# Kernel optimization log

Hardware: AMD Instinct MI355X
Metric: run time of the kernel (lower is better)

The kernel has to match this reference:

```python
import jax, jax.numpy as jnp
import numpy as np

N = 100000
E = 1600000
IN_DIM, HID, NCLS = 512, 64, 16


def setup_inputs() -> dict:
    key = jax.random.key(0)
    ks = jax.random.split(key, 6)
    x = jax.random.normal(ks[0], (N, IN_DIM), dtype=jnp.float32)
    edge_index = jax.random.randint(ks[1], (2, E), 0, N, dtype=jnp.int32)
    edge_weight = jax.random.uniform(ks[2], (E,), dtype=jnp.float32)
    W1 = jax.random.normal(ks[3], (IN_DIM, HID), dtype=jnp.float32) / np.sqrt(IN_DIM)
    b1 = jnp.zeros((HID,), dtype=jnp.float32)
    W2 = jax.random.normal(ks[4], (HID, NCLS), dtype=jnp.float32) / np.sqrt(HID)
    b2 = jnp.zeros((NCLS,), dtype=jnp.float32)
    return {"x": x, "edge_index": edge_index, "edge_weight": edge_weight,
            "W1": W1, "b1": b1, "W2": W2, "b2": b2}


def _gcn_norm(edge_index, edge_weight, num_nodes):
    # PyG GCNConv: add self-loops (weight 1), symmetric deg^-1/2 normalization.
    loop = jnp.arange(num_nodes, dtype=edge_index.dtype)
    src = jnp.concatenate([edge_index[0], loop])
    dst = jnp.concatenate([edge_index[1], loop])
    w = jnp.concatenate([edge_weight, jnp.ones((num_nodes,), edge_weight.dtype)])
    deg = jax.ops.segment_sum(w, dst, num_segments=num_nodes)  # degree at target
    dis = jnp.where(deg > 0, jax.lax.rsqrt(jnp.where(deg > 0, deg, 1.0)), 0.0)
    norm = dis[src] * w * dis[dst]
    return src, dst, norm


def _gcn_layer(x, src, dst, norm, W, b):
    h = x @ W                                   # [N, out]
    msg = h[src] * norm[:, None]                # gather + scale  [E+N, out]
    out = jax.ops.segment_sum(msg, dst, num_segments=x.shape[0])
    return out + b


def reference(x, edge_index, edge_weight, W1, b1, W2, b2):
    src, dst, norm = _gcn_norm(edge_index, edge_weight, x.shape[0])
    h = _gcn_layer(x, src, dst, norm, W1, b1)
    h = jax.nn.relu(h)
    # F.dropout in eval mode is identity (reference assumes inference).
    h = _gcn_layer(h, src, dst, norm, W2, b2)
    return jax.nn.log_softmax(h, axis=-1)
```

## Files before the change

kernel.cpp:

```cpp
#include <hip/hip_runtime.h>
#include <hip/hip_bf16.h>

#define N_NODES 100000
#define N_EDGES 1600000
#define IN_DIM 512
#define HID 64
#define NCLS 16
#define NB ((N_NODES + 1023) / 1024)

typedef __attribute__((ext_vector_type(8))) short bf16x8;
typedef __attribute__((ext_vector_type(8))) unsigned short ushort8;
typedef __attribute__((ext_vector_type(4))) float f32x4;

static __device__ __forceinline__ unsigned short f2bf(float f) {
    union { float f; unsigned int u; } v; v.f = f;
    unsigned int u = v.u;
    unsigned int r = (u + 0x7fffu + ((u >> 16) & 1u)) >> 16;
    return (unsigned short)r;
}
static __device__ __forceinline__ float bf2f(unsigned short u) {
    union { unsigned int i; float f; } v; v.i = ((unsigned int)u) << 16; return v.f;
}


__global__ void k_init(int* cnt) {
    int i = blockIdx.x * 256 + threadIdx.x;
    if (i < N_NODES) cnt[i] = 0;
}

__global__ void k_pass1(const int* __restrict__ dst, int* cnt, int* __restrict__ li) {
    int e = blockIdx.x * 256 + threadIdx.x;
    if (e < N_EDGES) li[e] = atomicAdd(&cnt[dst[e]], 1);
}

__global__ void k_scan1(const int* __restrict__ cnt, int* ptr, int* bsum) {
    __shared__ int s[256];
    int t = threadIdx.x;
    int i0 = blockIdx.x * 1024 + t * 4;
    int c[4];
#pragma unroll
    for (int j = 0; j < 4; j++) c[j] = (i0 + j < N_NODES) ? cnt[i0 + j] : 0;
    int sum4 = c[0] + c[1] + c[2] + c[3];
    s[t] = sum4;
    __syncthreads();
    int v = sum4;
    for (int off = 1; off < 256; off <<= 1) {
        int add = (t >= off) ? s[t - off] : 0;
        __syncthreads();
        v += add;
        s[t] = v;
        __syncthreads();
    }
    int run = v - sum4;
#pragma unroll
    for (int j = 0; j < 4; j++) {
        if (i0 + j < N_NODES) ptr[i0 + j] = run;
        run += c[j];
    }
    if (t == 255) bsum[blockIdx.x] = v;
}

__global__ void k_scan2(int* bsum, int* ptr) {
    __shared__ int s[128];
    int t = threadIdx.x;
    int val = (t < NB) ? bsum[t] : 0;
    s[t] = val;
    __syncthreads();
    int v = val;
    for (int off = 1; off < 128; off <<= 1) {
        int add = (t >= off) ? s[t - off] : 0;
        __syncthreads();
        v += add;
        s[t] = v;
        __syncthreads();
    }
    if (t < NB) bsum[t] = v - val;
    if (t == 0) ptr[N_NODES] = N_EDGES;
}

__global__ void k_scan3(int* ptr, const int* __restrict__ bsum) {
    int t = threadIdx.x;
    int i0 = blockIdx.x * 1024 + t * 4;
    int add = bsum[blockIdx.x];
#pragma unroll
    for (int j = 0; j < 4; j++)
        if (i0 + j < N_NODES) ptr[i0 + j] += add;
}

__global__ void k_pass2(const int* __restrict__ src, const int* __restrict__ dst,
                        const float* __restrict__ w, const int* __restrict__ ptr,
                        const int* __restrict__ li,
                        int* __restrict__ csr_src, float* __restrict__ csr_w) {
    int e = blockIdx.x * 256 + threadIdx.x;
    if (e < N_EDGES) {
        int p = ptr[dst[e]] + li[e];
        csr_src[p] = src[e];
        csr_w[p] = w[e];
    }
}

__global__ void k_degsum(const int* __restrict__ ptr, const float* __restrict__ csr_w,
                         float* __restrict__ dis) {
    int v = blockIdx.x * 256 + threadIdx.x;
    if (v < N_NODES) {
        int p0 = ptr[v], p1 = ptr[v + 1];
        float s = 1.0f;
        for (int p = p0; p < p1; p++) s += csr_w[p];
        dis[v] = rsqrtf(s);
    }
}

__global__ void k_scale(const int* __restrict__ ptr, const int* __restrict__ csr_src,
                        float* __restrict__ csr_w, const float* __restrict__ dis) {
    int v = blockIdx.x * 256 + threadIdx.x;
    if (v < N_NODES) {
        float dv = dis[v];
        int p0 = ptr[v], p1 = ptr[v + 1];
        for (int p = p0; p < p1; p++)
            csr_w[p] = csr_w[p] * dv * dis[csr_src[p]];
    }
}


__global__ void k_prep_w1(const float* __restrict__ W1, unsigned short* __restrict__ wt) {
    int t = blockIdx.x * 256 + threadIdx.x;
    if (t < HID * IN_DIM) {
        int n = t >> 9, k = t & 511;
        wt[t] = f2bf(W1[(size_t)k * HID + n]);
    }
}


#define LDK 72

__global__ __launch_bounds__(256) void k_gemm1(const float* __restrict__ x,
                                               const unsigned short* __restrict__ wt,
                                               unsigned short* __restrict__ h1b) {
    __shared__ unsigned short xs[64][LDK];
    __shared__ unsigned short ws[64][LDK];

    int t = threadIdx.x;
    int row0 = blockIdx.x * 64;
    int wave = t >> 6, lane = t & 63;
    int lm = lane & 15, quad = lane >> 4;

    f32x4 acc[4];
#pragma unroll
    for (int nt = 0; nt < 4; nt++) acc[nt] = (f32x4)(0.f);

    for (int k0 = 0; k0 < IN_DIM; k0 += 64) {
        __syncthreads();
        {
            int c8 = (t & 7) * 8;
#pragma unroll
            for (int h = 0; h < 2; h++) {
                int r = (t >> 3) + h * 32;
                int gr = row0 + r;
                if (gr >= N_NODES) gr = N_NODES - 1;
                const float* xp = x + (size_t)gr * IN_DIM + k0 + c8;
                float4 v0 = *(const float4*)xp;
                float4 v1 = *(const float4*)(xp + 4);
                ushort8 pk;
                pk.s0 = f2bf(v0.x); pk.s1 = f2bf(v0.y); pk.s2 = f2bf(v0.z); pk.s3 = f2bf(v0.w);
                pk.s4 = f2bf(v1.x); pk.s5 = f2bf(v1.y); pk.s6 = f2bf(v1.z); pk.s7 = f2bf(v1.w);
                *(ushort8*)&xs[r][c8] = pk;
            }
        }
        {
            int n = t >> 2, kc = (t & 3) * 16;
            const unsigned short* wp = wt + (size_t)n * IN_DIM + k0 + kc;
            *(ushort8*)&ws[n][kc]     = *(const ushort8*)wp;
            *(ushort8*)&ws[n][kc + 8] = *(const ushort8*)(wp + 8);
        }
        __syncthreads();
#pragma unroll
        for (int kk = 0; kk < 64; kk += 32) {
            bf16x8 afrag = *(bf16x8*)&xs[wave * 16 + lm][kk + quad * 8];
#pragma unroll
            for (int nt = 0; nt < 4; nt++) {
                bf16x8 bfrag = *(bf16x8*)&ws[nt * 16 + lm][kk + quad * 8];
                acc[nt] = __builtin_amdgcn_mfma_f32_16x16x32_bf16(afrag, bfrag, acc[nt], 0, 0, 0);
            }
        }
    }
#pragma unroll
    for (int nt = 0; nt < 4; nt++) {
#pragma unroll
        for (int i = 0; i < 4; i++) {
            int gr = row0 + wave * 16 + quad * 4 + i;
            if (gr < N_NODES) h1b[(size_t)gr * HID + nt * 16 + lm] = f2bf(acc[nt][i]);
        }
    }
}


__global__ __launch_bounds__(256) void k_agg1(const unsigned short* __restrict__ h1b,
                                              const int* __restrict__ ptr,
                                              const int* __restrict__ csr_src,
                                              const float* __restrict__ csr_w,
                                              const float* __restrict__ dis,
                                              const float* __restrict__ b1,
                                              float* __restrict__ a1) {
    int wave = threadIdx.x >> 6, lane = threadIdx.x & 63;
    int v = blockIdx.x * 4 + wave;
    if (v >= N_NODES) return;
    int j = lane >> 4, c = lane & 15;
    int p0 = ptr[v], p1 = ptr[v + 1];

    float a0 = 0.f, a1r = 0.f, a2 = 0.f, a3 = 0.f;
    for (int base = p0; base < p1; base += 8) {
#pragma unroll
        for (int half = 0; half < 2; half++) {
            int idx = base + half * 4 + j;
            bool valid = idx < p1;
            int s = valid ? csr_src[idx] : v;
            float wgt = valid ? csr_w[idx] : 0.f;
            ushort4 g = *(const ushort4*)&h1b[(size_t)s * HID + c * 4];
            a0 += wgt * bf2f(g.x);
            a1r += wgt * bf2f(g.y);
            a2 += wgt * bf2f(g.z);
            a3 += wgt * bf2f(g.w);
        }
    }
#pragma unroll
    for (int m = 16; m <= 32; m <<= 1) {
        a0 += __shfl_xor(a0, m, 64);
        a1r += __shfl_xor(a1r, m, 64);
        a2 += __shfl_xor(a2, m, 64);
        a3 += __shfl_xor(a3, m, 64);
    }
    if (lane < 16) {
        float dv = dis[v], dvv = dv * dv;
        ushort4 sv = *(const ushort4*)&h1b[(size_t)v * HID + c * 4];
        float4 bv = *(const float4*)&b1[c * 4];
        float r0 = a0 + dvv * bf2f(sv.x) + bv.x;
        float r1 = a1r + dvv * bf2f(sv.y) + bv.y;
        float r2 = a2 + dvv * bf2f(sv.z) + bv.z;
        float r3 = a3 + dvv * bf2f(sv.w) + bv.w;
        float4 o;
        o.x = r0 > 0.f ? r0 : 0.f;
        o.y = r1 > 0.f ? r1 : 0.f;
        o.z = r2 > 0.f ? r2 : 0.f;
        o.w = r3 > 0.f ? r3 : 0.f;
        *(float4*)&a1[(size_t)v * HID + c * 4] = o;
    }
}


__global__ __launch_bounds__(256) void k_gemm2(const float* __restrict__ a1,
                                               const float* __restrict__ W2,
                                               float* __restrict__ h2) {
    __shared__ float ws[HID * NCLS];
    for (int i = threadIdx.x; i < HID * NCLS; i += 256) ws[i] = W2[i];
    __syncthreads();
    int t = blockIdx.x * 256 + threadIdx.x;
    int v = t >> 4, c = t & 15;
    if (v >= N_NODES) return;
    const float* row = a1 + (size_t)v * HID;
    float acc = 0.f;
#pragma unroll
    for (int k = 0; k < HID; k += 4) {
        float4 av = *(const float4*)(row + k);
        acc = fmaf(av.x, ws[(k + 0) * NCLS + c], acc);
        acc = fmaf(av.y, ws[(k + 1) * NCLS + c], acc);
        acc = fmaf(av.z, ws[(k + 2) * NCLS + c], acc);
        acc = fmaf(av.w, ws[(k + 3) * NCLS + c], acc);
    }
    h2[(size_t)v * NCLS + c] = acc;
}


__global__ __launch_bounds__(256) void k_agg2(const float* __restrict__ h2,
                                              const int* __restrict__ ptr,
                                              const int* __restrict__ csr_src,
                                              const float* __restrict__ csr_w,
                                              const float* __restrict__ dis,
                                              const float* __restrict__ b2,
                                              float* __restrict__ out) {
    int t = blockIdx.x * 256 + threadIdx.x;
    int v = t >> 4, c = t & 15;
    if (v >= N_NODES) return;
    float dv = dis[v];
    float acc = h2[(size_t)v * NCLS + c] * dv * dv;
    int p0 = ptr[v], p1 = ptr[v + 1];
    int p = p0;
    int n4 = p0 + ((p1 - p0) & ~3);
    for (; p < n4; p += 4) {
        int s0 = csr_src[p], s1 = csr_src[p + 1], s2 = csr_src[p + 2], s3 = csr_src[p + 3];
        float w0 = csr_w[p], w1 = csr_w[p + 1], w2 = csr_w[p + 2], w3 = csr_w[p + 3];
        float g0 = h2[(size_t)s0 * NCLS + c];
        float g1 = h2[(size_t)s1 * NCLS + c];
        float g2 = h2[(size_t)s2 * NCLS + c];
        float g3 = h2[(size_t)s3 * NCLS + c];
        acc += w0 * g0 + w1 * g1 + w2 * g2 + w3 * g3;
    }
    for (; p < p1; p++)
        acc += csr_w[p] * h2[(size_t)csr_src[p] * NCLS + c];
    acc += b2[c];
    float m = acc;
#pragma unroll
    for (int off = 8; off >= 1; off >>= 1) m = fmaxf(m, __shfl_xor(m, off, 16));
    float e = expf(acc - m);
    float s = e;
#pragma unroll
    for (int off = 8; off >= 1; off >>= 1) s += __shfl_xor(s, off, 16);
    out[(size_t)v * NCLS + c] = acc - m - logf(s);
}


extern "C" void kernel_launch(void* const* d_in, const int* in_sizes, int n_in,
                              void* d_out, int out_size, void* d_ws, size_t ws_size,
                              hipStream_t stream) {
    const float* x  = (const float*)d_in[0];
    const int*   ei = (const int*)d_in[1];
    const float* w  = (const float*)d_in[2];
    const float* W1 = (const float*)d_in[3];
    const float* b1 = (const float*)d_in[4];
    const float* W2 = (const float*)d_in[5];
    const float* b2 = (const float*)d_in[6];
    const int* src = ei;
    const int* dst = ei + N_EDGES;

    char* wsb = (char*)d_ws;
    size_t off = 0;
    auto alloc = [&](size_t bytes) {
        void* p = wsb + off;
        off += (bytes + 255) & ~(size_t)255;
        return p;
    };
    int*   cnt   = (int*)  alloc((size_t)N_NODES * 4);
    int*   li    = (int*)  alloc((size_t)N_EDGES * 4);
    int*   ptr   = (int*)  alloc((size_t)(N_NODES + 1) * 4);
    int*   bsum  = (int*)  alloc((size_t)NB * 4);
    int*   csr_s = (int*)  alloc((size_t)N_EDGES * 4);
    float* csr_w = (float*)alloc((size_t)N_EDGES * 4);
    float* dis   = (float*)alloc((size_t)N_NODES * 4);
    unsigned short* h1b = (unsigned short*)alloc((size_t)N_NODES * HID * 2);
    float* a1    = (float*)alloc((size_t)N_NODES * HID * 4);
    float* h2    = (float*)alloc((size_t)N_NODES * NCLS * 4);
    unsigned short* wt = (unsigned short*)alloc((size_t)HID * IN_DIM * 2);

    float* outp = (float*)d_out;

    k_init   <<<(N_NODES + 255) / 256, 256, 0, stream>>>(cnt);
    k_pass1  <<<(N_EDGES + 255) / 256, 256, 0, stream>>>(dst, cnt, li);
    k_scan1  <<<NB, 256, 0, stream>>>(cnt, ptr, bsum);
    k_scan2  <<<1, 128, 0, stream>>>(bsum, ptr);
    k_scan3  <<<NB, 256, 0, stream>>>(ptr, bsum);
    k_pass2  <<<(N_EDGES + 255) / 256, 256, 0, stream>>>(src, dst, w, ptr, li, csr_s, csr_w);
    k_degsum <<<(N_NODES + 255) / 256, 256, 0, stream>>>(ptr, csr_w, dis);
    k_scale  <<<(N_NODES + 255) / 256, 256, 0, stream>>>(ptr, csr_s, csr_w, dis);
    k_prep_w1<<<(HID * IN_DIM + 255) / 256, 256, 0, stream>>>(W1, wt);
    k_gemm1  <<<(N_NODES + 63) / 64, 256, 0, stream>>>(x, wt, h1b);
    k_agg1   <<<(N_NODES + 3) / 4, 256, 0, stream>>>(h1b, ptr, csr_s, csr_w, dis, b1, a1);
    k_gemm2  <<<(N_NODES * NCLS + 255) / 256, 256, 0, stream>>>(a1, W2, h2);
    k_agg2   <<<(N_NODES * NCLS + 255) / 256, 256, 0, stream>>>(h2, ptr, csr_s, csr_w, dis, b2, outp);
}
```

Before: 579.8 us.

## Fold symmetric normalization into features and fuse GEMM2 into layer-1 aggregation

Drops the per-edge k_scale pass by pre-scaling node features by deg^-1/2 in the GEMM epilogues and applying the destination factor after aggregation. The second linear layer is fused into the layer-1 aggregation kernel through an LDS-resident transposed W2 and shuffle reductions, so the fp32 a1 intermediate is never written. Layer-2 features are stored as bf16 and aggregated with the same wave-per-node scheme as layer 1. This cuts memory traffic and one kernel launch, but adds bf16 rounding on h2 and more shuffle work in k_agg1.

```diff
diff --git a/kernel.cpp b/kernel.cpp
--- a/kernel.cpp
+++ b/kernel.cpp
@@ -110,17 +110,6 @@
     }
 }
 
-__global__ void k_scale(const int* __restrict__ ptr, const int* __restrict__ csr_src,
-                        float* __restrict__ csr_w, const float* __restrict__ dis) {
-    int v = blockIdx.x * 256 + threadIdx.x;
-    if (v < N_NODES) {
-        float dv = dis[v];
-        int p0 = ptr[v], p1 = ptr[v + 1];
-        for (int p = p0; p < p1; p++)
-            csr_w[p] = csr_w[p] * dv * dis[csr_src[p]];
-    }
-}
-
 
 __global__ void k_prep_w1(const float* __restrict__ W1, unsigned short* __restrict__ wt) {
     int t = blockIdx.x * 256 + threadIdx.x;
@@ -135,7 +124,8 @@
 
 __global__ __launch_bounds__(256) void k_gemm1(const float* __restrict__ x,
                                                const unsigned short* __restrict__ wt,
-                                               unsigned short* __restrict__ h1b) {
+                                               const float* __restrict__ dis,
+                                               unsigned short* __restrict__ h1s) {
     __shared__ unsigned short xs[64][LDK];
     __shared__ unsigned short ws[64][LDK];
 
@@ -184,30 +174,40 @@
         }
     }
 #pragma unroll
-    for (int nt = 0; nt < 4; nt++) {
-#pragma unroll
-        for (int i = 0; i < 4; i++) {
-            int gr = row0 + wave * 16 + quad * 4 + i;
-            if (gr < N_NODES) h1b[(size_t)gr * HID + nt * 16 + lm] = f2bf(acc[nt][i]);
-        }
-    }
-}
-
-
-__global__ __launch_bounds__(256) void k_agg1(const unsigned short* __restrict__ h1b,
+    for (int i = 0; i < 4; i++) {
+        int gr = row0 + wave * 16 + quad * 4 + i;
+        if (gr < N_NODES) {
+            float dv = dis[gr];
+#pragma unroll
+            for (int nt = 0; nt < 4; nt++)
+                h1s[(size_t)gr * HID + nt * 16 + lm] = f2bf(dv * acc[nt][i]);
+        }
+    }
+}
+
+
+__global__ __launch_bounds__(256) void k_agg1(const unsigned short* __restrict__ h1s,
                                               const int* __restrict__ ptr,
                                               const int* __restrict__ csr_src,
                                               const float* __restrict__ csr_w,
                                               const float* __restrict__ dis,
                                               const float* __restrict__ b1,
-                                              float* __restrict__ a1) {
+                                              const float* __restrict__ W2,
+                                              unsigned short* __restrict__ h2s) {
+    __shared__ float w2t[NCLS * 68];
+    for (int i = threadIdx.x; i < HID * NCLS; i += 256) {
+        int k = i >> 4, cc = i & 15;
+        w2t[cc * 68 + k] = W2[i];
+    }
+    __syncthreads();
+
     int wave = threadIdx.x >> 6, lane = threadIdx.x & 63;
     int v = blockIdx.x * 4 + wave;
     if (v >= N_NODES) return;
     int j = lane >> 4, c = lane & 15;
     int p0 = ptr[v], p1 = ptr[v + 1];
 
-    float a0 = 0.f, a1r = 0.f, a2 = 0.f, a3 = 0.f;
+    float a0 = 0.f, a1v = 0.f, a2 = 0.f, a3 = 0.f;
     for (int base = p0; base < p1; base += 8) {
 #pragma unroll
         for (int half = 0; half < 2; half++) {
@@ -215,9 +215,9 @@
             bool valid = idx < p1;
             int s = valid ? csr_src[idx] : v;
             float wgt = valid ? csr_w[idx] : 0.f;
-            ushort4 g = *(const ushort4*)&h1b[(size_t)s * HID + c * 4];
+            ushort4 g = *(const ushort4*)&h1s[(size_t)s * HID + c * 4];
             a0 += wgt * bf2f(g.x);
-            a1r += wgt * bf2f(g.y);
+            a1v += wgt * bf2f(g.y);
             a2 += wgt * bf2f(g.z);
             a3 += wgt * bf2f(g.w);
         }
@@ -225,86 +225,81 @@
 #pragma unroll
     for (int m = 16; m <= 32; m <<= 1) {
         a0 += __shfl_xor(a0, m, 64);
-        a1r += __shfl_xor(a1r, m, 64);
+        a1v += __shfl_xor(a1v, m, 64);
         a2 += __shfl_xor(a2, m, 64);
         a3 += __shfl_xor(a3, m, 64);
     }
+    float dv = dis[v];
+    ushort4 sv = *(const ushort4*)&h1s[(size_t)v * HID + c * 4];
+    float4 bv = *(const float4*)&b1[c * 4];
+    float r0 = dv * (a0 + bf2f(sv.x)) + bv.x;
+    float r1 = dv * (a1v + bf2f(sv.y)) + bv.y;
+    float r2 = dv * (a2 + bf2f(sv.z)) + bv.z;
+    float r3 = dv * (a3 + bf2f(sv.w)) + bv.w;
+    r0 = r0 > 0.f ? r0 : 0.f;
+    r1 = r1 > 0.f ? r1 : 0.f;
+    r2 = r2 > 0.f ? r2 : 0.f;
+    r3 = r3 > 0.f ? r3 : 0.f;
+
+    float partial[NCLS];
+#pragma unroll
+    for (int cc = 0; cc < NCLS; cc++) {
+        const float* wp = &w2t[cc * 68 + 4 * c];
+        partial[cc] = r0 * wp[0] + r1 * wp[1] + r2 * wp[2] + r3 * wp[3];
+    }
+#pragma unroll
+    for (int m = 1; m <= 8; m <<= 1)
+#pragma unroll
+        for (int cc = 0; cc < NCLS; cc++)
+            partial[cc] += __shfl_xor(partial[cc], m, 16);
+
     if (lane < 16) {
-        float dv = dis[v], dvv = dv * dv;
-        ushort4 sv = *(const ushort4*)&h1b[(size_t)v * HID + c * 4];
-        float4 bv = *(const float4*)&b1[c * 4];
-        float r0 = a0 + dvv * bf2f(sv.x) + bv.x;
-        float r1 = a1r + dvv * bf2f(sv.y) + bv.y;
-        float r2 = a2 + dvv * bf2f(sv.z) + bv.z;
-        float r3 = a3 + dvv * bf2f(sv.w) + bv.w;
-        float4 o;
-        o.x = r0 > 0.f ? r0 : 0.f;
-        o.y = r1 > 0.f ? r1 : 0.f;
-        o.z = r2 > 0.f ? r2 : 0.f;
-        o.w = r3 > 0.f ? r3 : 0.f;
-        *(float4*)&a1[(size_t)v * HID + c * 4] = o;
-    }
-}
-
-
-__global__ __launch_bounds__(256) void k_gemm2(const float* __restrict__ a1,
-                                               const float* __restrict__ W2,
-                                               float* __restrict__ h2) {
-    __shared__ float ws[HID * NCLS];
-    for (int i = threadIdx.x; i < HID * NCLS; i += 256) ws[i] = W2[i];
-    __syncthreads();
-    int t = blockIdx.x * 256 + threadIdx.x;
-    int v = t >> 4, c = t & 15;
-    if (v >= N_NODES) return;
-    const float* row = a1 + (size_t)v * HID;
-    float acc = 0.f;
-#pragma unroll
-    for (int k = 0; k < HID; k += 4) {
-        float4 av = *(const float4*)(row + k);
-        acc = fmaf(av.x, ws[(k + 0) * NCLS + c], acc);
-        acc = fmaf(av.y, ws[(k + 1) * NCLS + c], acc);
-        acc = fmaf(av.z, ws[(k + 2) * NCLS + c], acc);
-        acc = fmaf(av.w, ws[(k + 3) * NCLS + c], acc);
-    }
-    h2[(size_t)v * NCLS + c] = acc;
-}
-
-
-__global__ __launch_bounds__(256) void k_agg2(const float* __restrict__ h2,
+        float sel = partial[0];
+#pragma unroll
+        for (int cc = 1; cc < NCLS; cc++) sel = (c == cc) ? partial[cc] : sel;
+        h2s[(size_t)v * NCLS + c] = f2bf(dv * sel);
+    }
+}
+
+
+__global__ __launch_bounds__(256) void k_agg2(const unsigned short* __restrict__ h2s,
                                               const int* __restrict__ ptr,
                                               const int* __restrict__ csr_src,
                                               const float* __restrict__ csr_w,
                                               const float* __restrict__ dis,
                                               const float* __restrict__ b2,
                                               float* __restrict__ out) {
-    int t = blockIdx.x * 256 + threadIdx.x;
-    int v = t >> 4, c = t & 15;
+    int wave = threadIdx.x >> 6, lane = threadIdx.x & 63;
+    int v = blockIdx.x * 4 + wave;
     if (v >= N_NODES) return;
+    int j = lane >> 4, c = lane & 15;
+    int p0 = ptr[v], p1 = ptr[v + 1];
+
+    float acc = 0.f;
+    for (int base = p0; base < p1; base += 8) {
+#pragma unroll
+        for (int half = 0; half < 2; half++) {
+            int idx = base + half * 4 + j;
+            bool valid = idx < p1;
+            int s = valid ? csr_src[idx] : v;
+            float wgt = valid ? csr_w[idx] : 0.f;
+            acc += wgt * bf2f(h2s[(size_t)s * NCLS + c]);
+        }
+    }
+#pragma unroll
+    for (int m = 16; m <= 32; m <<= 1) acc += __shfl_xor(acc, m, 64);
+
     float dv = dis[v];
-    float acc = h2[(size_t)v * NCLS + c] * dv * dv;
-    int p0 = ptr[v], p1 = ptr[v + 1];
-    int p = p0;
-    int n4 = p0 + ((p1 - p0) & ~3);
-    for (; p < n4; p += 4) {
-        int s0 = csr_src[p], s1 = csr_src[p + 1], s2 = csr_src[p + 2], s3 = csr_src[p + 3];
-        float w0 = csr_w[p], w1 = csr_w[p + 1], w2 = csr_w[p + 2], w3 = csr_w[p + 3];
-        float g0 = h2[(size_t)s0 * NCLS + c];
-        float g1 = h2[(size_t)s1 * NCLS + c];
-        float g2 = h2[(size_t)s2 * NCLS + c];
-        float g3 = h2[(size_t)s3 * NCLS + c];
-        acc += w0 * g0 + w1 * g1 + w2 * g2 + w3 * g3;
-    }
-    for (; p < p1; p++)
-        acc += csr_w[p] * h2[(size_t)csr_src[p] * NCLS + c];
-    acc += b2[c];
-    float m = acc;
-#pragma unroll
-    for (int off = 8; off >= 1; off >>= 1) m = fmaxf(m, __shfl_xor(m, off, 16));
-    float e = expf(acc - m);
+    float z = dv * (acc + bf2f(h2s[(size_t)v * NCLS + c])) + b2[c];
+
+    float mx = z;
+#pragma unroll
+    for (int off = 8; off >= 1; off >>= 1) mx = fmaxf(mx, __shfl_xor(mx, off, 16));
+    float e = expf(z - mx);
     float s = e;
 #pragma unroll
     for (int off = 8; off >= 1; off >>= 1) s += __shfl_xor(s, off, 16);
-    out[(size_t)v * NCLS + c] = acc - m - logf(s);
+    if (lane < 16) out[(size_t)v * NCLS + c] = z - mx - logf(s);
 }
 
 
@@ -335,10 +330,9 @@
     int*   csr_s = (int*)  alloc((size_t)N_EDGES * 4);
     float* csr_w = (float*)alloc((size_t)N_EDGES * 4);
     float* dis   = (float*)alloc((size_t)N_NODES * 4);
-    unsigned short* h1b = (unsigned short*)alloc((size_t)N_NODES * HID * 2);
-    float* a1    = (float*)alloc((size_t)N_NODES * HID * 4);
-    float* h2    = (float*)alloc((size_t)N_NODES * NCLS * 4);
-    unsigned short* wt = (unsigned short*)alloc((size_t)HID * IN_DIM * 2);
+    unsigned short* h1s = (unsigned short*)alloc((size_t)N_NODES * HID * 2);
+    unsigned short* h2s = (unsigned short*)alloc((size_t)N_NODES * NCLS * 2);
+    unsigned short* wt  = (unsigned short*)alloc((size_t)HID * IN_DIM * 2);
 
     float* outp = (float*)d_out;
 
@@ -349,10 +343,8 @@
     k_scan3  <<<NB, 256, 0, stream>>>(ptr, bsum);
     k_pass2  <<<(N_EDGES + 255) / 256, 256, 0, stream>>>(src, dst, w, ptr, li, csr_s, csr_w);
     k_degsum <<<(N_NODES + 255) / 256, 256, 0, stream>>>(ptr, csr_w, dis);
-    k_scale  <<<(N_NODES + 255) / 256, 256, 0, stream>>>(ptr, csr_s, csr_w, dis);
     k_prep_w1<<<(HID * IN_DIM + 255) / 256, 256, 0, stream>>>(W1, wt);
-    k_gemm1  <<<(N_NODES + 63) / 64, 256, 0, stream>>>(x, wt, h1b);
-    k_agg1   <<<(N_NODES + 3) / 4, 256, 0, stream>>>(h1b, ptr, csr_s, csr_w, dis, b1, a1);
-    k_gemm2  <<<(N_NODES * NCLS + 255) / 256, 256, 0, stream>>>(a1, W2, h2);
-    k_agg2   <<<(N_NODES * NCLS + 255) / 256, 256, 0, stream>>>(h2, ptr, csr_s, csr_w, dis, b2, outp);
-}
+    k_gemm1  <<<(N_NODES + 63) / 64, 256, 0, stream>>>(x, wt, dis, h1s);
+    k_agg1   <<<(N_NODES + 3) / 4, 256, 0, stream>>>(h1s, ptr, csr_s, csr_w, dis, b1, W2, h2s);
+    k_agg2   <<<(N_NODES + 3) / 4, 256, 0, stream>>>(h2s, ptr, csr_s, csr_w, dis, b2, outp);
+}
```

Measured after the change: 621.2 us. 7.1% more time.
